# Optimization experiments

Hardware: AMD Instinct MI355X
Metric: run time of the kernel (lower is better)

## Reference

```python
import jax, jax.numpy as jnp
import numpy as np

B, C, W, H = 16, 256, 32, 32  # L = W*H = 1024
NUM_HEAD = 4
DIM_HEAD = C  # dim_head defaults to in_channels


def setup_inputs() -> dict:
    key = jax.random.key(0)
    ks = jax.random.split(key, 6)
    s = 0.02  # small init scale, like trained linear weights
    return {
        "x": jax.random.normal(ks[0], (B, C, W, H), dtype=jnp.float32),
        "Wq": jax.random.normal(ks[1], (NUM_HEAD, DIM_HEAD, C), dtype=jnp.float32) * s,
        "Wk": jax.random.normal(ks[2], (NUM_HEAD, DIM_HEAD, C), dtype=jnp.float32) * s,
        "Wv": jax.random.normal(ks[3], (NUM_HEAD, DIM_HEAD, C), dtype=jnp.float32) * s,
        "Wo_w": jax.random.normal(ks[4], (C, NUM_HEAD * DIM_HEAD), dtype=jnp.float32) * s,
        "Wo_b": jax.random.normal(ks[5], (C,), dtype=jnp.float32) * s,
    }


def reference(x, Wq, Wk, Wv, Wo_w, Wo_b):
    b, c, w, h = x.shape
    L = w * h
    # [b,c,w,h] -> [b,L,c]
    xs = jnp.transpose(x, (0, 2, 3, 1)).reshape(b, L, c)
    # per-head projections (torch Linear: y = x @ W^T), batched over heads
    Q = jnp.einsum('blc,hdc->bhld', xs, Wq)
    K = jnp.einsum('blc,hdc->bhld', xs, Wk)
    V = jnp.einsum('blc,hdc->bhld', xs, Wv)
    # no softmax: scores = Q K^T, heads = scores V
    scores = jnp.einsum('bhld,bhmd->bhlm', Q, K)  # [b,H,L,L]
    heads = jnp.einsum('bhlm,bhmd->bhld', scores, V)  # [b,H,L,d]
    # concat heads along channel dim -> [b,L,H*d], then output projection
    cat = jnp.transpose(heads, (0, 2, 1, 3)).reshape(b, L, -1)
    z = cat @ Wo_w.T + Wo_b  # [b,L,c]
    return jnp.transpose(z, (0, 2, 1)).reshape(b, c, w, h)
```

## Files before the change

kernel.cpp:

```cpp
#include <hip/hip_runtime.h>
#include <hip/hip_bf16.h>

typedef __attribute__((ext_vector_type(8))) short s8v;
typedef __attribute__((ext_vector_type(4))) float f4v;

__device__ __forceinline__ ushort f2bf(float f) {
    unsigned u = __builtin_bit_cast(unsigned, f);
    unsigned r = (u + 0x7fffu + ((u >> 16) & 1u)) >> 16;
    return (ushort)r;
}

__device__ __forceinline__ int fsw(int row) { return ((row >> 1) ^ (row >> 3)) & 3; }

__device__ __forceinline__ void gload16(const ushort* g, ushort* l) {
    __builtin_amdgcn_global_load_lds(
        (const __attribute__((address_space(1))) unsigned*)g,
        (__attribute__((address_space(3))) unsigned*)l, 16, 0, 0);
}

__device__ __forceinline__ void cvtw16(ushort* p, float4 a, float4 b) {
    s8v u;
    u[0] = (short)f2bf(a.x); u[1] = (short)f2bf(a.y);
    u[2] = (short)f2bf(a.z); u[3] = (short)f2bf(a.w);
    u[4] = (short)f2bf(b.x); u[5] = (short)f2bf(b.y);
    u[6] = (short)f2bf(b.z); u[7] = (short)f2bf(b.w);
    *(s8v*)p = u;
}

__device__ __forceinline__ void scatw(ushort* L, int c8, int d, float4 a, float4 b) {
    float v[8] = { a.x, a.y, a.z, a.w, b.x, b.y, b.z, b.w };
#pragma unroll
    for (int i = 0; i < 8; ++i) {
        int row = c8 + i;
        L[row * 32 + (((d >> 3) ^ fsw(row)) << 3) + (d & 7)] = f2bf(v[i]);
    }
}

template<int NT>
__device__ __forceinline__ void gemmS(
    const float* __restrict__ Xb, const float* __restrict__ Yb,
    ushort* lds, int row0, int col0, ushort* __restrict__ O, int ldo) {
    const int tid = threadIdx.x, wave = tid >> 6, lane = tid & 63;
    const int g = wave >> 2, w4 = wave & 3;
    const int wr = w4 >> 1, wc = w4 & 1;
    const int rA = lane & 15, kg = lane >> 4;
    const int tg = tid & 255;
    const int srow = tg >> 2, slot = tg & 3;
    const int kb = g * (NT * 32);
    ushort* LA = lds + g * 16384;
    ushort* LB = LA + 8192;
    const int wadr = srow * 32 + ((slot ^ fsw(srow)) << 3);
    const float* gx = Xb + (size_t)(row0 + srow) * 1024 + kb + slot * 8;
    const float* gy = Yb + (size_t)(col0 + srow) * 1024 + kb + slot * 8;
    f4v acc[2][2] = {};

    float4 bx[4][2], by[4][2];
#pragma unroll
    for (int p = 0; p < 3; ++p) {
        bx[p][0] = *(const float4*)(gx + p * 32);
        bx[p][1] = *(const float4*)(gx + p * 32 + 4);
        by[p][0] = *(const float4*)(gy + p * 32);
        by[p][1] = *(const float4*)(gy + p * 32 + 4);
    }
    cvtw16(LA + wadr, bx[0][0], bx[0][1]);
    cvtw16(LB + wadr, by[0][0], by[0][1]);

#pragma unroll
    for (int t = 0; t < NT; ++t) {
        if (t + 3 < NT) {
            const int bi = (t + 3) & 3;
            bx[bi][0] = *(const float4*)(gx + (t + 3) * 32);
            bx[bi][1] = *(const float4*)(gx + (t + 3) * 32 + 4);
            by[bi][0] = *(const float4*)(gy + (t + 3) * 32);
            by[bi][1] = *(const float4*)(gy + (t + 3) * 32 + 4);
        }
        if (t + 1 < NT) {
            const int bi = (t + 1) & 3;
            cvtw16(LA + ((t + 1) & 3) * 2048 + wadr, bx[bi][0], bx[bi][1]);
            cvtw16(LB + ((t + 1) & 3) * 2048 + wadr, by[bi][0], by[bi][1]);
        }
        asm volatile("s_waitcnt lgkmcnt(0)" ::: "memory");
        __builtin_amdgcn_s_barrier();
        __builtin_amdgcn_sched_barrier(0);
        const ushort* pa = LA + (t & 3) * 2048;
        const ushort* pb = LB + (t & 3) * 2048;
        s8v a[2], b[2];
#pragma unroll
        for (int m = 0; m < 2; ++m) {
            int row = wr * 32 + m * 16 + rA;
            a[m] = *(const s8v*)&pa[row * 32 + ((kg ^ fsw(row)) << 3)];
        }
#pragma unroll
        for (int n = 0; n < 2; ++n) {
            int row = wc * 32 + n * 16 + rA;
            b[n] = *(const s8v*)&pb[row * 32 + ((kg ^ fsw(row)) << 3)];
        }
#pragma unroll
        for (int m = 0; m < 2; ++m)
#pragma unroll
            for (int n = 0; n < 2; ++n)
                acc[m][n] = __builtin_amdgcn_mfma_f32_16x16x32_bf16(a[m], b[n], acc[m][n], 0, 0, 0);
    }
    __syncthreads();
    float* red = (float*)lds;
    if (g == 1) {
#pragma unroll
        for (int m = 0; m < 2; ++m)
#pragma unroll
            for (int n = 0; n < 2; ++n)
                *(f4v*)&red[(w4 * 64 + lane) * 16 + (m * 2 + n) * 4] = acc[m][n];
    }
    __syncthreads();
    if (g == 0) {
        int r4 = (lane >> 4) * 4, cl = lane & 15;
#pragma unroll
        for (int m = 0; m < 2; ++m)
#pragma unroll
            for (int n = 0; n < 2; ++n) {
                f4v o = *(const f4v*)&red[(w4 * 64 + lane) * 16 + (m * 2 + n) * 4];
                f4v s = acc[m][n] + o;
                int row = row0 + wr * 32 + m * 16 + r4;
                int col = col0 + wc * 32 + n * 16 + cl;
#pragma unroll
                for (int r = 0; r < 4; ++r)
                    O[(size_t)(row + r) * ldo + col] = f2bf(s[r]);
            }
    }
}

template<int XT>
__device__ __forceinline__ void gemmWT(
    const float* __restrict__ Xw, const float* __restrict__ Yw,
    ushort* lds, int row0, int col0, ushort* __restrict__ O, int ldo) {
    const int NT = 4;
    const int tid = threadIdx.x, wave = tid >> 6, lane = tid & 63;
    const int g = wave >> 2, w4 = wave & 3;
    const int wr = w4 >> 1, wc = w4 & 1;
    const int rA = lane & 15, kg = lane >> 4;
    const int tg = tid & 255;
    const int kb = g * 128;
    ushort* LA = lds + g * 16384;
    ushort* LB = LA + 8192;
    const int dT = tg >> 3, c8 = (tg & 7) * 8;
    const int srow = tg >> 2, slot = tg & 3;
    const int wadr = srow * 32 + ((slot ^ fsw(srow)) << 3);
    f4v acc[2][2] = {};

    float4 bx[4][2], by[4][2];
#pragma unroll
    for (int p = 0; p < 3; ++p) {
        if (XT) {
            bx[p][0] = *(const float4*)(Xw + (size_t)(kb + p * 32 + dT) * 256 + row0 + c8);
            bx[p][1] = *(const float4*)(Xw + (size_t)(kb + p * 32 + dT) * 256 + row0 + c8 + 4);
        } else {
            bx[p][0] = *(const float4*)(Xw + (size_t)(row0 + srow) * 1024 + kb + p * 32 + slot * 8);
            bx[p][1] = *(const float4*)(Xw + (size_t)(row0 + srow) * 1024 + kb + p * 32 + slot * 8 + 4);
        }
        by[p][0] = *(const float4*)(Yw + (size_t)(kb + p * 32 + dT) * 256 + col0 + c8);
        by[p][1] = *(const float4*)(Yw + (size_t)(kb + p * 32 + dT) * 256 + col0 + c8 + 4);
    }
    if (XT) scatw(LA, c8, dT, bx[0][0], bx[0][1]);
    else    cvtw16(LA + wadr, bx[0][0], bx[0][1]);
    scatw(LB, c8, dT, by[0][0], by[0][1]);

#pragma unroll
    for (int t = 0; t < NT; ++t) {
        if (t + 3 < NT) {
            const int bi = (t + 3) & 3;
            if (XT) {
                bx[bi][0] = *(const float4*)(Xw + (size_t)(kb + (t + 3) * 32 + dT) * 256 + row0 + c8);
                bx[bi][1] = *(const float4*)(Xw + (size_t)(kb + (t + 3) * 32 + dT) * 256 + row0 + c8 + 4);
            } else {
                bx[bi][0] = *(const float4*)(Xw + (size_t)(row0 + srow) * 1024 + kb + (t + 3) * 32 + slot * 8);
                bx[bi][1] = *(const float4*)(Xw + (size_t)(row0 + srow) * 1024 + kb + (t + 3) * 32 + slot * 8 + 4);
            }
            by[bi][0] = *(const float4*)(Yw + (size_t)(kb + (t + 3) * 32 + dT) * 256 + col0 + c8);
            by[bi][1] = *(const float4*)(Yw + (size_t)(kb + (t + 3) * 32 + dT) * 256 + col0 + c8 + 4);
        }
        if (t + 1 < NT) {
            const int bi = (t + 1) & 3;
            ushort* la = LA + ((t + 1) & 3) * 2048;
            ushort* lb = LB + ((t + 1) & 3) * 2048;
            if (XT) scatw(la, c8, dT, bx[bi][0], bx[bi][1]);
            else    cvtw16(la + wadr, bx[bi][0], bx[bi][1]);
            scatw(lb, c8, dT, by[bi][0], by[bi][1]);
        }
        asm volatile("s_waitcnt lgkmcnt(0)" ::: "memory");
        __builtin_amdgcn_s_barrier();
        __builtin_amdgcn_sched_barrier(0);
        const ushort* pa = LA + (t & 3) * 2048;
        const ushort* pb = LB + (t & 3) * 2048;
        s8v a[2], b[2];
#pragma unroll
        for (int m = 0; m < 2; ++m) {
            int row = wr * 32 + m * 16 + rA;
            a[m] = *(const s8v*)&pa[row * 32 + ((kg ^ fsw(row)) << 3)];
        }
#pragma unroll
        for (int n = 0; n < 2; ++n) {
            int row = wc * 32 + n * 16 + rA;
            b[n] = *(const s8v*)&pb[row * 32 + ((kg ^ fsw(row)) << 3)];
        }
#pragma unroll
        for (int m = 0; m < 2; ++m)
#pragma unroll
            for (int n = 0; n < 2; ++n)
                acc[m][n] = __builtin_amdgcn_mfma_f32_16x16x32_bf16(a[m], b[n], acc[m][n], 0, 0, 0);
    }
    __syncthreads();
    float* red = (float*)lds;
    if (g == 1) {
#pragma unroll
        for (int m = 0; m < 2; ++m)
#pragma unroll
            for (int n = 0; n < 2; ++n)
                *(f4v*)&red[(w4 * 64 + lane) * 16 + (m * 2 + n) * 4] = acc[m][n];
    }
    __syncthreads();
    if (g == 0) {
        int r4 = (lane >> 4) * 4, cl = lane & 15;
#pragma unroll
        for (int m = 0; m < 2; ++m)
#pragma unroll
            for (int n = 0; n < 2; ++n) {
                f4v o = *(const f4v*)&red[(w4 * 64 + lane) * 16 + (m * 2 + n) * 4];
                f4v s = acc[m][n] + o;
                int row = row0 + wr * 32 + m * 16 + r4;
                int col = col0 + wc * 32 + n * 16 + cl;
#pragma unroll
                for (int r = 0; r < 4; ++r)
                    O[(size_t)(row + r) * ldo + col] = f2bf(s[r]);
            }
    }
}

__device__ __forceinline__ void gemm64x8(
    const ushort* __restrict__ Xb, const ushort* __restrict__ Yb,
    int ldx, int ldy, ushort* lds, int row0, int col0, int K,
    ushort* __restrict__ O, int ldo) {
    const int tid = threadIdx.x, wave = tid >> 6, lane = tid & 63;
    const int g = wave >> 2, w4 = wave & 3;
    const int wr = w4 >> 1, wc = w4 & 1;
    const int rA = lane & 15, kg = lane >> 4;
    const int srow = w4 * 16 + (lane >> 2);
    const int scol = ((lane & 3) ^ fsw(srow)) * 8;
    const int K2 = K >> 1, NT = K2 >> 5, kb = g * K2;
    ushort* LA = lds + g * 16384;
    ushort* LB = LA + 8192;
    f4v acc[2][2] = {};
    __syncthreads();
    const ushort* gx = Xb + (size_t)(row0 + srow) * ldx + kb + scol;
    const ushort* gy = Yb + (size_t)(col0 + srow) * ldy + kb + scol;
    gload16(gx,      LA + w4 * 512);
    gload16(gy,      LB + w4 * 512);
    gload16(gx + 32, LA + 2048 + w4 * 512);
    gload16(gy + 32, LB + 2048 + w4 * 512);
    for (int t = 0; t < NT; ++t) {
        if (t + 2 < NT) {
            int s2 = (t + 2) & 3, kt = (t + 2) << 5;
            gload16(gx + kt, LA + s2 * 2048 + w4 * 512);
            gload16(gy + kt, LB + s2 * 2048 + w4 * 512);
            asm volatile("s_waitcnt vmcnt(4)" ::: "memory");
        } else if (t + 1 < NT) {
            asm volatile("s_waitcnt vmcnt(2)" ::: "memory");
        } else {
            asm volatile("s_waitcnt vmcnt(0)" ::: "memory");
        }
        __builtin_amdgcn_s_barrier();
        __builtin_amdgcn_sched_barrier(0);
        const ushort* pa = LA + (t & 3) * 2048;
        const ushort* pb = LB + (t & 3) * 2048;
        s8v a[2], b[2];
#pragma unroll
        for (int m = 0; m < 2; ++m) {
            int row = wr * 32 + m * 16 + rA;
            a[m] = *(const s8v*)&pa[row * 32 + ((kg ^ fsw(row)) << 3)];
        }
#pragma unroll
        for (int n = 0; n < 2; ++n) {
            int row = wc * 32 + n * 16 + rA;
            b[n] = *(const s8v*)&pb[row * 32 + ((kg ^ fsw(row)) << 3)];
        }
#pragma unroll
        for (int m = 0; m < 2; ++m)
#pragma unroll
            for (int n = 0; n < 2; ++n)
                acc[m][n] = __builtin_amdgcn_mfma_f32_16x16x32_bf16(a[m], b[n], acc[m][n], 0, 0, 0);
    }
    __syncthreads();
    float* red = (float*)lds;
    if (g == 1) {
#pragma unroll
        for (int m = 0; m < 2; ++m)
#pragma unroll
            for (int n = 0; n < 2; ++n)
                *(f4v*)&red[(w4 * 64 + lane) * 16 + (m * 2 + n) * 4] = acc[m][n];
    }
    __syncthreads();
    if (g == 0) {
        int r4 = (lane >> 4) * 4, cl = lane & 15;
#pragma unroll
        for (int m = 0; m < 2; ++m)
#pragma unroll
            for (int n = 0; n < 2; ++n) {
                f4v o = *(const f4v*)&red[(w4 * 64 + lane) * 16 + (m * 2 + n) * 4];
                f4v s = acc[m][n] + o;
                int row = row0 + wr * 32 + m * 16 + r4;
                int col = col0 + wc * 32 + n * 16 + cl;
#pragma unroll
                for (int r = 0; r < 4; ++r)
                    O[(size_t)(row + r) * ldo + col] = f2bf(s[r]);
            }
    }
}

template<int OBF>
__device__ __forceinline__ void gemm128x8(
    const ushort* __restrict__ Xb, const ushort* __restrict__ Yb,
    int ldx, int ldy, ushort* lds, int row0, int col0, int K,
    void* __restrict__ Oraw, int ldo, const float* __restrict__ bias) {
    const int tid = threadIdx.x, wave = tid >> 6, lane = tid & 63;
    const int wr = wave >> 2, wc = wave & 3;
    const int rA = lane & 15, kg = lane >> 4;
    const int srow = wave * 16 + (lane >> 2);
    const int scol = ((lane & 3) ^ fsw(srow)) * 8;
    const int NT = K >> 5;
    ushort* LA = lds;
    ushort* LB = lds + 16384;
    f4v acc[4][2] = {};
    __syncthreads();
    const ushort* gx = Xb + (size_t)(row0 + srow) * ldx + scol;
    const ushort* gy = Yb + (size_t)(col0 + srow) * ldy + scol;
#pragma unroll
    for (int p = 0; p < 2; ++p) {
        gload16(gx + p * 32, LA + p * 4096 + wave * 512);
        gload16(gy + p * 32, LB + p * 4096 + wave * 512);
    }
    for (int t = 0; t < NT; ++t) {
        if (t + 2 < NT) {
            int s2 = (t + 2) & 3, kt = (t + 2) << 5;
            gload16(gx + kt, LA + s2 * 4096 + wave * 512);
            gload16(gy + kt, LB + s2 * 4096 + wave * 512);
            asm volatile("s_waitcnt vmcnt(4)" ::: "memory");
        } else if (t + 1 < NT) {
            asm volatile("s_waitcnt vmcnt(2)" ::: "memory");
        } else {
            asm volatile("s_waitcnt vmcnt(0)" ::: "memory");
        }
        __builtin_amdgcn_s_barrier();
        __builtin_amdgcn_sched_barrier(0);
        const ushort* pa = LA + (t & 3) * 4096;
        const ushort* pb = LB + (t & 3) * 4096;
        s8v a[4], b[2];
#pragma unroll
        for (int m = 0; m < 4; ++m) {
            int row = wr * 64 + m * 16 + rA;
            a[m] = *(const s8v*)&pa[row * 32 + ((kg ^ fsw(row)) << 3)];
        }
#pragma unroll
        for (int n = 0; n < 2; ++n) {
            int row = wc * 32 + n * 16 + rA;
            b[n] = *(const s8v*)&pb[row * 32 + ((kg ^ fsw(row)) << 3)];
        }
#pragma unroll
        for (int m = 0; m < 4; ++m)
#pragma unroll
            for (int n = 0; n < 2; ++n)
                acc[m][n] = __builtin_amdgcn_mfma_f32_16x16x32_bf16(a[m], b[n], acc[m][n], 0, 0, 0);
    }
    int r4 = (lane >> 4) * 4, cl = lane & 15;
    if (OBF) {
        ushort* O = (ushort*)Oraw;
#pragma unroll
        for (int m = 0; m < 4; ++m)
#pragma unroll
            for (int n = 0; n < 2; ++n) {
                int row = row0 + wr * 64 + m * 16 + r4;
                int col = col0 + wc * 32 + n * 16 + cl;
#pragma unroll
                for (int r = 0; r < 4; ++r)
                    O[(size_t)(row + r) * ldo + col] = f2bf(acc[m][n][r]);
            }
    } else {
        float* O = (float*)Oraw;
#pragma unroll
        for (int m = 0; m < 4; ++m)
#pragma unroll
            for (int n = 0; n < 2; ++n) {
                int row = row0 + wr * 64 + m * 16 + r4;
                int col = col0 + wc * 32 + n * 16 + cl;
#pragma unroll
                for (int r = 0; r < 4; ++r)
                    O[(size_t)(row + r) * ldo + col] = acc[m][n][r] + bias[row + r];
            }
    }
}

__global__ __launch_bounds__(512, 2) void kSP(
    const float* __restrict__ x, const float* __restrict__ Wq,
    const float* __restrict__ Wk, const float* __restrict__ Wv,
    const float* __restrict__ Wo,
    ushort* __restrict__ xlc, ushort* __restrict__ S16,
    ushort* __restrict__ A16, ushort* __restrict__ BT) {
    __shared__ __align__(16) ushort lds[32768];
    const int bid = blockIdx.x, tid = threadIdx.x;
    {
        int xcd = bid & 7, idx = bid >> 3;
        int b = 2 * xcd + (idx >> 4), tile = idx & 15;
        const float* Xb = x + (size_t)b * 262144;
        gemmS<16>(Xb, Xb, lds, (tile >> 2) * 64, (tile & 3) * 64,
                  S16 + (size_t)b * 65536, 256);
    }
    for (int jid = bid; jid < 1152; jid += 256) {
        __syncthreads();
        if (jid < 1024) {
            ushort (*t)[72] = (ushort(*)[72])lds;
            int lt = jid & 15, ct = (jid >> 4) & 3, b2 = jid >> 6;
            int r = tid >> 3, c0 = (tid & 7) * 8;
            size_t so = (size_t)(b2 * 256 + ct * 64 + r) * 1024 + lt * 64 + c0;
            float4 v0 = *(const float4*)(x + so);
            float4 v1 = *(const float4*)(x + so + 4);
            ushort4 u0 = { f2bf(v0.x), f2bf(v0.y), f2bf(v0.z), f2bf(v0.w) };
            ushort4 u1 = { f2bf(v1.x), f2bf(v1.y), f2bf(v1.z), f2bf(v1.w) };
            *(ushort4*)&t[r][c0] = u0;
            *(ushort4*)&t[r][c0 + 4] = u1;
            __syncthreads();
            size_t dof = (size_t)(b2 * 1024 + lt * 64 + r) * 256 + ct * 64 + c0;
            ushort4 w0 = { t[c0][r], t[c0 + 1][r], t[c0 + 2][r], t[c0 + 3][r] };
            ushort4 w1 = { t[c0 + 4][r], t[c0 + 5][r], t[c0 + 6][r], t[c0 + 7][r] };
            *(ushort4*)(xlc + dof) = w0;
            *(ushort4*)(xlc + dof + 4) = w1;
        } else if (jid < 1088) {
            int q = jid - 1024, h = q >> 4, t2 = q & 15;
            gemmWT<1>(Wq + (size_t)h * 65536, Wk + (size_t)h * 65536, lds,
                      (t2 >> 2) * 64, (t2 & 3) * 64, A16 + (size_t)h * 65536, 256);
        } else {
            int q = jid - 1088, h = q >> 4, t2 = q & 15;
            gemmWT<0>(Wo + (size_t)h * 256, Wv + (size_t)h * 65536, lds,
                      (t2 >> 2) * 64, (t2 & 3) * 64, BT + (size_t)h * 256, 1024);
        }
    }
}

__global__ __launch_bounds__(512, 2) void kT1(
    const ushort* __restrict__ A16, const ushort* __restrict__ S16,
    ushort* __restrict__ T1) {
    __shared__ __align__(16) ushort lds[32768];
    int j = blockIdx.x, xcd = j & 7, idx = j >> 3;
    int b = 2 * xcd + (idx >> 4), h = (idx >> 2) & 3, tile = idx & 3;
    gemm128x8<1>(A16 + (size_t)h * 65536, S16 + (size_t)b * 65536, 256, 256, lds,
                 (tile >> 1) * 128, (tile & 1) * 128, 256,
                 T1 + (size_t)b * 262144 + h * 256, 1024, nullptr);
}

__global__ __launch_bounds__(512, 2) void kGT(
    const ushort* __restrict__ BT, const ushort* __restrict__ T1,
    ushort* __restrict__ GT) {
    __shared__ __align__(16) ushort lds[32768];
    int j = blockIdx.x, xcd = j & 7, idx = j >> 3;
    int b = 2 * xcd + (idx >> 4), tile = idx & 15;
    gemm64x8(BT, T1 + (size_t)b * 262144, 1024, 1024, lds,
             (tile >> 2) * 64, (tile & 3) * 64, 1024, GT + (size_t)b * 65536, 256);
}

__global__ __launch_bounds__(512, 2) void kOUT(
    const ushort* __restrict__ GT, const ushort* __restrict__ xlc,
    float* __restrict__ out, const float* __restrict__ bias) {
    __shared__ __align__(16) ushort lds[32768];
    int j = blockIdx.x, xcd = j & 7, idx = j >> 3;
    int b = 2 * xcd + (idx >> 4), tile = idx & 15;
    gemm128x8<0>(GT + (size_t)b * 65536, xlc + (size_t)b * 262144, 256, 256, lds,
                 (tile >> 3) * 128, (tile & 7) * 128, 256,
                 out + (size_t)b * 262144, 1024, bias);
}

extern "C" void kernel_launch(void* const* d_in, const int* in_sizes, int n_in,
                              void* d_out, int out_size, void* d_ws, size_t ws_size,
                              hipStream_t stream) {
    const float* x  = (const float*)d_in[0];
    const float* Wq = (const float*)d_in[1];
    const float* Wk = (const float*)d_in[2];
    const float* Wv = (const float*)d_in[3];
    const float* Wo = (const float*)d_in[4];
    const float* Wb = (const float*)d_in[5];

    char* ws = (char*)d_ws;
    ushort* xlc = (ushort*)(ws + 0);
    ushort* T1  = (ushort*)(ws + 8388608);
    ushort* S16 = (ushort*)(ws + 16777216);
    ushort* GT  = (ushort*)(ws + 18874368);
    ushort* A16 = (ushort*)(ws + 20971520);
    ushort* BT  = (ushort*)(ws + 21495808);

    hipLaunchKernelGGL(kSP,  dim3(256), dim3(512), 0, stream,
                       x, Wq, Wk, Wv, Wo, xlc, S16, A16, BT);
    hipLaunchKernelGGL(kT1,  dim3(256), dim3(512), 0, stream, A16, S16, T1);
    hipLaunchKernelGGL(kGT,  dim3(256), dim3(512), 0, stream, BT, T1, GT);
    hipLaunchKernelGGL(kOUT, dim3(256), dim3(512), 0, stream, GT, xlc, (float*)d_out, Wb);
}
```

Measured before the change: 42.83 us.

## Fuse four kernels into one persistent megakernel with per-batch atomic barriers

Replaces the four-kernel launch sequence with a single persistent kernel that uses global atomic flag counters as per-batch and weight-ready barriers between stages. This removes the inter-kernel launch gaps and the extra xlc transpose pass: the final GEMM reads the fp32 input directly and converts it to bf16 while staging into LDS. The bf16 conversion helper is also switched to the library intrinsic. The cost is spin-wait barriers that rely on all 256 blocks being co-resident, plus an added memset launch to clear the flags.

```diff
diff --git a/kernel.cpp b/kernel.cpp
--- a/kernel.cpp
+++ b/kernel.cpp
@@ -5,9 +5,8 @@
 typedef __attribute__((ext_vector_type(4))) float f4v;
 
 __device__ __forceinline__ ushort f2bf(float f) {
-    unsigned u = __builtin_bit_cast(unsigned, f);
-    unsigned r = (u + 0x7fffu + ((u >> 16) & 1u)) >> 16;
-    return (ushort)r;
+    __hip_bfloat16 h = __float2bfloat16(f);
+    return __builtin_bit_cast(ushort, h);
 }
 
 __device__ __forceinline__ int fsw(int row) { return ((row >> 1) ^ (row >> 3)) & 3; }
@@ -34,6 +33,25 @@
         int row = c8 + i;
         L[row * 32 + (((d >> 3) ^ fsw(row)) << 3) + (d & 7)] = f2bf(v[i]);
     }
+}
+
+__device__ __forceinline__ void barB(unsigned* flags, int idx, unsigned tgt,
+                                     int alsoIdx, unsigned alsoTgt) {
+    __syncthreads();
+    if (threadIdx.x == 0) {
+        __threadfence();
+        atomicAdd(&flags[idx], 1u);
+        for (;;) {
+            unsigned v = __hip_atomic_load(&flags[idx], __ATOMIC_RELAXED, __HIP_MEMORY_SCOPE_AGENT);
+            unsigned w = (alsoIdx >= 0)
+                ? __hip_atomic_load(&flags[alsoIdx], __ATOMIC_RELAXED, __HIP_MEMORY_SCOPE_AGENT)
+                : alsoTgt;
+            if (v >= tgt && w >= alsoTgt) break;
+            __builtin_amdgcn_s_sleep(2);
+        }
+        __threadfence();
+    }
+    __syncthreads();
 }
 
 template<int NT>
@@ -53,6 +71,7 @@
     const float* gx = Xb + (size_t)(row0 + srow) * 1024 + kb + slot * 8;
     const float* gy = Yb + (size_t)(col0 + srow) * 1024 + kb + slot * 8;
     f4v acc[2][2] = {};
+    __syncthreads();
 
     float4 bx[4][2], by[4][2];
 #pragma unroll
@@ -145,6 +164,7 @@
     const int srow = tg >> 2, slot = tg & 3;
     const int wadr = srow * 32 + ((slot ^ fsw(srow)) << 3);
     f4v acc[2][2] = {};
+    __syncthreads();
 
     float4 bx[4][2], by[4][2];
 #pragma unroll
@@ -314,11 +334,10 @@
     }
 }
 
-template<int OBF>
 __device__ __forceinline__ void gemm128x8(
     const ushort* __restrict__ Xb, const ushort* __restrict__ Yb,
     int ldx, int ldy, ushort* lds, int row0, int col0, int K,
-    void* __restrict__ Oraw, int ldo, const float* __restrict__ bias) {
+    ushort* __restrict__ O, int ldo) {
     const int tid = threadIdx.x, wave = tid >> 6, lane = tid & 63;
     const int wr = wave >> 2, wc = wave & 3;
     const int rA = lane & 15, kg = lane >> 4;
@@ -369,109 +388,159 @@
                 acc[m][n] = __builtin_amdgcn_mfma_f32_16x16x32_bf16(a[m], b[n], acc[m][n], 0, 0, 0);
     }
     int r4 = (lane >> 4) * 4, cl = lane & 15;
-    if (OBF) {
-        ushort* O = (ushort*)Oraw;
+    ushort* Ob = O;
+#pragma unroll
+    for (int m = 0; m < 4; ++m)
+#pragma unroll
+        for (int n = 0; n < 2; ++n) {
+            int row = row0 + wr * 64 + m * 16 + r4;
+            int col = col0 + wc * 32 + n * 16 + cl;
+#pragma unroll
+            for (int r = 0; r < 4; ++r)
+                Ob[(size_t)(row + r) * ldo + col] = f2bf(acc[m][n][r]);
+        }
+}
+
+__device__ __forceinline__ void gemmOUT(
+    const ushort* __restrict__ Ga, const float* __restrict__ Xf,
+    ushort* lds, int row0, int col0,
+    float* __restrict__ O, const float* __restrict__ bias) {
+    const int tid = threadIdx.x, wave = tid >> 6, lane = tid & 63;
+    const int wr = wave >> 2, wc = wave & 3;
+    const int rA = lane & 15, kg = lane >> 4;
+    const int srowA = wave * 16 + (lane >> 2);
+    const int scolA = ((lane & 3) ^ fsw(srowA)) * 8;
+    ushort* LA = lds;
+    ushort* LB = lds + 16384;
+    const int kk = tid >> 4, l8 = (tid & 15) * 8;
+    int wadr[8];
+#pragma unroll
+    for (int i = 0; i < 8; ++i) {
+        int row = l8 + i;
+        wadr[i] = row * 32 + (((kk >> 3) ^ fsw(row)) << 3) + (kk & 7);
+    }
+    const ushort* gA = Ga + (size_t)(row0 + srowA) * 256 + scolA;
+    const float* gB = Xf + (size_t)kk * 1024 + col0 + l8;
+    f4v acc[4][2] = {};
+    __syncthreads();
+
+    float4 ra[4], rb[4];
+    gload16(gA + 0, LA + 0 * 4096 + wave * 512);
+    ra[0] = *(const float4*)(gB);
+    rb[0] = *(const float4*)(gB + 4);
+    gload16(gA + 32, LA + 1 * 4096 + wave * 512);
+    ra[1] = *(const float4*)(gB + 32768);
+    rb[1] = *(const float4*)(gB + 32768 + 4);
+    asm volatile("s_waitcnt vmcnt(0)" ::: "memory");
+    {
+        float v[8] = { ra[0].x, ra[0].y, ra[0].z, ra[0].w, rb[0].x, rb[0].y, rb[0].z, rb[0].w };
+#pragma unroll
+        for (int i = 0; i < 8; ++i) LB[wadr[i]] = f2bf(v[i]);
+    }
+    asm volatile("s_waitcnt lgkmcnt(0)" ::: "memory");
+    __builtin_amdgcn_s_barrier();
+    __builtin_amdgcn_sched_barrier(0);
+
+#pragma unroll
+    for (int t = 0; t < 8; ++t) {
+        if (t + 1 < 8) {
+            if (t + 2 < 8) {
+                gload16(gA + (t + 2) * 32, LA + ((t + 2) & 3) * 4096 + wave * 512);
+                ra[(t + 2) & 3] = *(const float4*)(gB + (size_t)(t + 2) * 32768);
+                rb[(t + 2) & 3] = *(const float4*)(gB + (size_t)(t + 2) * 32768 + 4);
+            }
+            {
+                const int bi = (t + 1) & 3;
+                float v[8] = { ra[bi].x, ra[bi].y, ra[bi].z, ra[bi].w,
+                               rb[bi].x, rb[bi].y, rb[bi].z, rb[bi].w };
+                ushort* lb = LB + bi * 4096;
+#pragma unroll
+                for (int i = 0; i < 8; ++i) lb[wadr[i]] = f2bf(v[i]);
+            }
+            if (t + 2 < 8) { asm volatile("s_waitcnt vmcnt(3)" ::: "memory"); }
+            else           { asm volatile("s_waitcnt vmcnt(0)" ::: "memory"); }
+            asm volatile("s_waitcnt lgkmcnt(0)" ::: "memory");
+            __builtin_amdgcn_s_barrier();
+            __builtin_amdgcn_sched_barrier(0);
+        }
+        const ushort* pa = LA + (t & 3) * 4096;
+        const ushort* pb = LB + (t & 3) * 4096;
+        s8v a[4], b[2];
+#pragma unroll
+        for (int m = 0; m < 4; ++m) {
+            int row = wr * 64 + m * 16 + rA;
+            a[m] = *(const s8v*)&pa[row * 32 + ((kg ^ fsw(row)) << 3)];
+        }
+#pragma unroll
+        for (int n = 0; n < 2; ++n) {
+            int row = wc * 32 + n * 16 + rA;
+            b[n] = *(const s8v*)&pb[row * 32 + ((kg ^ fsw(row)) << 3)];
+        }
 #pragma unroll
         for (int m = 0; m < 4; ++m)
 #pragma unroll
-            for (int n = 0; n < 2; ++n) {
-                int row = row0 + wr * 64 + m * 16 + r4;
-                int col = col0 + wc * 32 + n * 16 + cl;
-#pragma unroll
-                for (int r = 0; r < 4; ++r)
-                    O[(size_t)(row + r) * ldo + col] = f2bf(acc[m][n][r]);
-            }
-    } else {
-        float* O = (float*)Oraw;
-#pragma unroll
-        for (int m = 0; m < 4; ++m)
-#pragma unroll
-            for (int n = 0; n < 2; ++n) {
-                int row = row0 + wr * 64 + m * 16 + r4;
-                int col = col0 + wc * 32 + n * 16 + cl;
-#pragma unroll
-                for (int r = 0; r < 4; ++r)
-                    O[(size_t)(row + r) * ldo + col] = acc[m][n][r] + bias[row + r];
-            }
-    }
-}
-
-__global__ __launch_bounds__(512, 2) void kSP(
+            for (int n = 0; n < 2; ++n)
+                acc[m][n] = __builtin_amdgcn_mfma_f32_16x16x32_bf16(a[m], b[n], acc[m][n], 0, 0, 0);
+    }
+    int r4 = (lane >> 4) * 4, cl = lane & 15;
+#pragma unroll
+    for (int m = 0; m < 4; ++m)
+#pragma unroll
+        for (int n = 0; n < 2; ++n) {
+            int row = row0 + wr * 64 + m * 16 + r4;
+            int col = col0 + wc * 32 + n * 16 + cl;
+#pragma unroll
+            for (int r = 0; r < 4; ++r)
+                O[(size_t)(row + r) * 1024 + col] = acc[m][n][r] + bias[row + r];
+        }
+}
+
+__global__ __launch_bounds__(512, 2) void mega(
     const float* __restrict__ x, const float* __restrict__ Wq,
     const float* __restrict__ Wk, const float* __restrict__ Wv,
-    const float* __restrict__ Wo,
-    ushort* __restrict__ xlc, ushort* __restrict__ S16,
-    ushort* __restrict__ A16, ushort* __restrict__ BT) {
+    const float* __restrict__ Wo, const float* __restrict__ Wb,
+    float* __restrict__ out,
+    ushort* __restrict__ T1, ushort* __restrict__ S16, ushort* __restrict__ GT,
+    ushort* __restrict__ A16, ushort* __restrict__ BT, unsigned* __restrict__ flags) {
     __shared__ __align__(16) ushort lds[32768];
     const int bid = blockIdx.x, tid = threadIdx.x;
-    {
-        int xcd = bid & 7, idx = bid >> 3;
-        int b = 2 * xcd + (idx >> 4), tile = idx & 15;
-        const float* Xb = x + (size_t)b * 262144;
-        gemmS<16>(Xb, Xb, lds, (tile >> 2) * 64, (tile & 3) * 64,
-                  S16 + (size_t)b * 65536, 256);
-    }
-    for (int jid = bid; jid < 1152; jid += 256) {
-        __syncthreads();
-        if (jid < 1024) {
-            ushort (*t)[72] = (ushort(*)[72])lds;
-            int lt = jid & 15, ct = (jid >> 4) & 3, b2 = jid >> 6;
-            int r = tid >> 3, c0 = (tid & 7) * 8;
-            size_t so = (size_t)(b2 * 256 + ct * 64 + r) * 1024 + lt * 64 + c0;
-            float4 v0 = *(const float4*)(x + so);
-            float4 v1 = *(const float4*)(x + so + 4);
-            ushort4 u0 = { f2bf(v0.x), f2bf(v0.y), f2bf(v0.z), f2bf(v0.w) };
-            ushort4 u1 = { f2bf(v1.x), f2bf(v1.y), f2bf(v1.z), f2bf(v1.w) };
-            *(ushort4*)&t[r][c0] = u0;
-            *(ushort4*)&t[r][c0 + 4] = u1;
-            __syncthreads();
-            size_t dof = (size_t)(b2 * 1024 + lt * 64 + r) * 256 + ct * 64 + c0;
-            ushort4 w0 = { t[c0][r], t[c0 + 1][r], t[c0 + 2][r], t[c0 + 3][r] };
-            ushort4 w1 = { t[c0 + 4][r], t[c0 + 5][r], t[c0 + 6][r], t[c0 + 7][r] };
-            *(ushort4*)(xlc + dof) = w0;
-            *(ushort4*)(xlc + dof + 4) = w1;
-        } else if (jid < 1088) {
-            int q = jid - 1024, h = q >> 4, t2 = q & 15;
+
+    if (bid < 128) {
+        if (bid < 64) {
+            int h = bid >> 4, t2 = bid & 15;
             gemmWT<1>(Wq + (size_t)h * 65536, Wk + (size_t)h * 65536, lds,
                       (t2 >> 2) * 64, (t2 & 3) * 64, A16 + (size_t)h * 65536, 256);
         } else {
-            int q = jid - 1088, h = q >> 4, t2 = q & 15;
+            int q = bid - 64, h = q >> 4, t2 = q & 15;
             gemmWT<0>(Wo + (size_t)h * 256, Wv + (size_t)h * 65536, lds,
                       (t2 >> 2) * 64, (t2 & 3) * 64, BT + (size_t)h * 256, 1024);
         }
-    }
-}
-
-__global__ __launch_bounds__(512, 2) void kT1(
-    const ushort* __restrict__ A16, const ushort* __restrict__ S16,
-    ushort* __restrict__ T1) {
-    __shared__ __align__(16) ushort lds[32768];
-    int j = blockIdx.x, xcd = j & 7, idx = j >> 3;
-    int b = 2 * xcd + (idx >> 4), h = (idx >> 2) & 3, tile = idx & 3;
-    gemm128x8<1>(A16 + (size_t)h * 65536, S16 + (size_t)b * 65536, 256, 256, lds,
-                 (tile >> 1) * 128, (tile & 1) * 128, 256,
-                 T1 + (size_t)b * 262144 + h * 256, 1024, nullptr);
-}
-
-__global__ __launch_bounds__(512, 2) void kGT(
-    const ushort* __restrict__ BT, const ushort* __restrict__ T1,
-    ushort* __restrict__ GT) {
-    __shared__ __align__(16) ushort lds[32768];
-    int j = blockIdx.x, xcd = j & 7, idx = j >> 3;
-    int b = 2 * xcd + (idx >> 4), tile = idx & 15;
+        __syncthreads();
+        if (tid == 0) { __threadfence(); atomicAdd(&flags[48], 1u); }
+    }
+
+    const int xcd = bid & 7;
+    const int b = 2 * xcd + ((bid >> 3) & 1);
+    const int t = bid >> 4;
+    const float* xb = x + (size_t)b * 262144;
+
+    gemmS<16>(xb, xb, lds, (t >> 2) * 64, (t & 3) * 64, S16 + (size_t)b * 65536, 256);
+    barB(flags, b * 3 + 0, 16, 48, 128);
+
+    {
+        int h = t >> 2, q = t & 3;
+        gemm128x8(A16 + (size_t)h * 65536, S16 + (size_t)b * 65536, 256, 256, lds,
+                  (q >> 1) * 128, (q & 1) * 128, 256,
+                  T1 + (size_t)b * 262144 + h * 256, 1024);
+    }
+    barB(flags, b * 3 + 1, 16, -1, 0);
+
     gemm64x8(BT, T1 + (size_t)b * 262144, 1024, 1024, lds,
-             (tile >> 2) * 64, (tile & 3) * 64, 1024, GT + (size_t)b * 65536, 256);
-}
-
-__global__ __launch_bounds__(512, 2) void kOUT(
-    const ushort* __restrict__ GT, const ushort* __restrict__ xlc,
-    float* __restrict__ out, const float* __restrict__ bias) {
-    __shared__ __align__(16) ushort lds[32768];
-    int j = blockIdx.x, xcd = j & 7, idx = j >> 3;
-    int b = 2 * xcd + (idx >> 4), tile = idx & 15;
-    gemm128x8<0>(GT + (size_t)b * 65536, xlc + (size_t)b * 262144, 256, 256, lds,
-                 (tile >> 3) * 128, (tile & 7) * 128, 256,
-                 out + (size_t)b * 262144, 1024, bias);
+             (t >> 2) * 64, (t & 3) * 64, 1024, GT + (size_t)b * 65536, 256);
+    barB(flags, b * 3 + 2, 16, -1, 0);
+
+    gemmOUT(GT + (size_t)b * 65536, xb, lds,
+            (t >> 3) * 128, (t & 7) * 128, out + (size_t)b * 262144, Wb);
 }
 
 extern "C" void kernel_launch(void* const* d_in, const int* in_sizes, int n_in,
@@ -485,16 +554,15 @@
     const float* Wb = (const float*)d_in[5];
 
     char* ws = (char*)d_ws;
-    ushort* xlc = (ushort*)(ws + 0);
-    ushort* T1  = (ushort*)(ws + 8388608);
-    ushort* S16 = (ushort*)(ws + 16777216);
-    ushort* GT  = (ushort*)(ws + 18874368);
-    ushort* A16 = (ushort*)(ws + 20971520);
-    ushort* BT  = (ushort*)(ws + 21495808);
-
-    hipLaunchKernelGGL(kSP,  dim3(256), dim3(512), 0, stream,
-                       x, Wq, Wk, Wv, Wo, xlc, S16, A16, BT);
-    hipLaunchKernelGGL(kT1,  dim3(256), dim3(512), 0, stream, A16, S16, T1);
-    hipLaunchKernelGGL(kGT,  dim3(256), dim3(512), 0, stream, BT, T1, GT);
-    hipLaunchKernelGGL(kOUT, dim3(256), dim3(512), 0, stream, GT, xlc, (float*)d_out, Wb);
-}
+    ushort*   T1    = (ushort*)(ws + 0);
+    ushort*   S16   = (ushort*)(ws + 16777216);
+    ushort*   GT    = (ushort*)(ws + 20971520);
+    ushort*   A16   = (ushort*)(ws + 25165824);
+    ushort*   BT    = (ushort*)(ws + 26214400);
+    unsigned* flags = (unsigned*)(ws + 33554432);
+
+    hipMemsetAsync(flags, 0, 256, stream);
+    hipLaunchKernelGGL(mega, dim3(256), dim3(512), 0, stream,
+                       x, Wq, Wk, Wv, Wo, Wb, (float*)d_out,
+                       T1, S16, GT, A16, BT, flags);
+}
```

Result: slower. 100.8 us (+135.3%).

## Exploit Gram symmetry, split projection prep into separate blocks, move Wo·Wv to kT1

Applied to the files above, without the earlier changes.

The x·x^T Gram matrix is symmetric, so only the upper-triangle 64x64 tiles are computed (10 of 16 per batch) and each off-diagonal tile is also written transposed. The kSP grid becomes 480 blocks with distinct roles (Gram tiles, Wq·Wk products, x transpose), so they no longer share one looped schedule. The Wo·Wv product moves into kT1 as extra blocks, which shortens the first kernel. The bf16 conversion now uses the library intrinsic, and the mirror writes are scattered 8-byte stores that may be poorly coalesced.

```diff
diff --git a/kernel.cpp b/kernel.cpp
--- a/kernel.cpp
+++ b/kernel.cpp
@@ -5,9 +5,8 @@
 typedef __attribute__((ext_vector_type(4))) float f4v;
 
 __device__ __forceinline__ ushort f2bf(float f) {
-    unsigned u = __builtin_bit_cast(unsigned, f);
-    unsigned r = (u + 0x7fffu + ((u >> 16) & 1u)) >> 16;
-    return (ushort)r;
+    __hip_bfloat16 h = __float2bfloat16(f);
+    return __builtin_bit_cast(ushort, h);
 }
 
 __device__ __forceinline__ int fsw(int row) { return ((row >> 1) ^ (row >> 3)) & 3; }
@@ -36,10 +35,10 @@
     }
 }
 
-template<int NT>
 __device__ __forceinline__ void gemmS(
-    const float* __restrict__ Xb, const float* __restrict__ Yb,
-    ushort* lds, int row0, int col0, ushort* __restrict__ O, int ldo) {
+    const float* __restrict__ Xb, ushort* lds, int row0, int col0,
+    ushort* __restrict__ S, int mirror) {
+    const int NT = 16;
     const int tid = threadIdx.x, wave = tid >> 6, lane = tid & 63;
     const int g = wave >> 2, w4 = wave & 3;
     const int wr = w4 >> 1, wc = w4 & 1;
@@ -51,8 +50,9 @@
     ushort* LB = LA + 8192;
     const int wadr = srow * 32 + ((slot ^ fsw(srow)) << 3);
     const float* gx = Xb + (size_t)(row0 + srow) * 1024 + kb + slot * 8;
-    const float* gy = Yb + (size_t)(col0 + srow) * 1024 + kb + slot * 8;
+    const float* gy = Xb + (size_t)(col0 + srow) * 1024 + kb + slot * 8;
     f4v acc[2][2] = {};
+    __syncthreads();
 
     float4 bx[4][2], by[4][2];
 #pragma unroll
@@ -121,9 +121,13 @@
                 f4v s = acc[m][n] + o;
                 int row = row0 + wr * 32 + m * 16 + r4;
                 int col = col0 + wc * 32 + n * 16 + cl;
-#pragma unroll
-                for (int r = 0; r < 4; ++r)
-                    O[(size_t)(row + r) * ldo + col] = f2bf(s[r]);
+                ushort4 tv = { f2bf(s[0]), f2bf(s[1]), f2bf(s[2]), f2bf(s[3]) };
+                S[(size_t)(row + 0) * 256 + col] = tv.x;
+                S[(size_t)(row + 1) * 256 + col] = tv.y;
+                S[(size_t)(row + 2) * 256 + col] = tv.z;
+                S[(size_t)(row + 3) * 256 + col] = tv.w;
+                if (mirror)
+                    *(ushort4*)&S[(size_t)col * 256 + row] = tv;
             }
     }
 }
@@ -145,6 +149,7 @@
     const int srow = tg >> 2, slot = tg & 3;
     const int wadr = srow * 32 + ((slot ^ fsw(srow)) << 3);
     f4v acc[2][2] = {};
+    __syncthreads();
 
     float4 bx[4][2], by[4][2];
 #pragma unroll
@@ -398,25 +403,33 @@
 
 __global__ __launch_bounds__(512, 2) void kSP(
     const float* __restrict__ x, const float* __restrict__ Wq,
-    const float* __restrict__ Wk, const float* __restrict__ Wv,
-    const float* __restrict__ Wo,
-    ushort* __restrict__ xlc, ushort* __restrict__ S16,
-    ushort* __restrict__ A16, ushort* __restrict__ BT) {
+    const float* __restrict__ Wk,
+    ushort* __restrict__ S16, ushort* __restrict__ A16, ushort* __restrict__ xlc) {
     __shared__ __align__(16) ushort lds[32768];
     const int bid = blockIdx.x, tid = threadIdx.x;
-    {
+    if (bid < 160) {
         int xcd = bid & 7, idx = bid >> 3;
-        int b = 2 * xcd + (idx >> 4), tile = idx & 15;
-        const float* Xb = x + (size_t)b * 262144;
-        gemmS<16>(Xb, Xb, lds, (tile >> 2) * 64, (tile & 3) * 64,
-                  S16 + (size_t)b * 65536, 256);
-    }
-    for (int jid = bid; jid < 1152; jid += 256) {
-        __syncthreads();
-        if (jid < 1024) {
-            ushort (*t)[72] = (ushort(*)[72])lds;
+        int b = 2 * xcd + (idx >= 10);
+        int tri = (idx >= 10) ? idx - 10 : idx;
+        int ti, tj;
+        if (tri < 4)      { ti = 0; tj = tri; }
+        else if (tri < 7) { ti = 1; tj = tri - 3; }
+        else if (tri < 9) { ti = 2; tj = tri - 5; }
+        else              { ti = 3; tj = 3; }
+        const float* xb = x + (size_t)b * 262144;
+        gemmS(xb, lds, ti * 64, tj * 64, S16 + (size_t)b * 65536, ti != tj);
+    } else if (bid < 224) {
+        int q = bid - 160, h = q >> 4, t2 = q & 15;
+        gemmWT<1>(Wq + (size_t)h * 65536, Wk + (size_t)h * 65536, lds,
+                  (t2 >> 2) * 64, (t2 & 3) * 64, A16 + (size_t)h * 65536, 256);
+    } else {
+        ushort (*t)[72] = (ushort(*)[72])lds;
+        int r = tid >> 3, c0 = (tid & 7) * 8;
+#pragma unroll
+        for (int rr = 0; rr < 4; ++rr) {
+            int jid = (bid - 224) + 256 * rr;
+            __syncthreads();
             int lt = jid & 15, ct = (jid >> 4) & 3, b2 = jid >> 6;
-            int r = tid >> 3, c0 = (tid & 7) * 8;
             size_t so = (size_t)(b2 * 256 + ct * 64 + r) * 1024 + lt * 64 + c0;
             float4 v0 = *(const float4*)(x + so);
             float4 v1 = *(const float4*)(x + so + 4);
@@ -430,27 +443,27 @@
             ushort4 w1 = { t[c0 + 4][r], t[c0 + 5][r], t[c0 + 6][r], t[c0 + 7][r] };
             *(ushort4*)(xlc + dof) = w0;
             *(ushort4*)(xlc + dof + 4) = w1;
-        } else if (jid < 1088) {
-            int q = jid - 1024, h = q >> 4, t2 = q & 15;
-            gemmWT<1>(Wq + (size_t)h * 65536, Wk + (size_t)h * 65536, lds,
-                      (t2 >> 2) * 64, (t2 & 3) * 64, A16 + (size_t)h * 65536, 256);
-        } else {
-            int q = jid - 1088, h = q >> 4, t2 = q & 15;
-            gemmWT<0>(Wo + (size_t)h * 256, Wv + (size_t)h * 65536, lds,
-                      (t2 >> 2) * 64, (t2 & 3) * 64, BT + (size_t)h * 256, 1024);
         }
     }
 }
 
 __global__ __launch_bounds__(512, 2) void kT1(
     const ushort* __restrict__ A16, const ushort* __restrict__ S16,
-    ushort* __restrict__ T1) {
+    const float* __restrict__ Wo, const float* __restrict__ Wv,
+    ushort* __restrict__ T1, ushort* __restrict__ BT) {
     __shared__ __align__(16) ushort lds[32768];
-    int j = blockIdx.x, xcd = j & 7, idx = j >> 3;
-    int b = 2 * xcd + (idx >> 4), h = (idx >> 2) & 3, tile = idx & 3;
-    gemm128x8<1>(A16 + (size_t)h * 65536, S16 + (size_t)b * 65536, 256, 256, lds,
-                 (tile >> 1) * 128, (tile & 1) * 128, 256,
-                 T1 + (size_t)b * 262144 + h * 256, 1024, nullptr);
+    int j = blockIdx.x;
+    if (j < 256) {
+        int xcd = j & 7, idx = j >> 3;
+        int b = 2 * xcd + (idx >> 4), h = (idx >> 2) & 3, tile = idx & 3;
+        gemm128x8<1>(A16 + (size_t)h * 65536, S16 + (size_t)b * 65536, 256, 256, lds,
+                     (tile >> 1) * 128, (tile & 1) * 128, 256,
+                     T1 + (size_t)b * 262144 + h * 256, 1024, nullptr);
+    } else {
+        int q = j - 256, h = q >> 4, t2 = q & 15;
+        gemmWT<0>(Wo + (size_t)h * 256, Wv + (size_t)h * 65536, lds,
+                  (t2 >> 2) * 64, (t2 & 3) * 64, BT + (size_t)h * 256, 1024);
+    }
 }
 
 __global__ __launch_bounds__(512, 2) void kGT(
@@ -485,16 +498,15 @@
     const float* Wb = (const float*)d_in[5];
 
     char* ws = (char*)d_ws;
-    ushort* xlc = (ushort*)(ws + 0);
-    ushort* T1  = (ushort*)(ws + 8388608);
+    ushort* T1  = (ushort*)(ws + 0);
+    ushort* xlc = (ushort*)(ws + 8388608);
     ushort* S16 = (ushort*)(ws + 16777216);
-    ushort* GT  = (ushort*)(ws + 18874368);
-    ushort* A16 = (ushort*)(ws + 20971520);
-    ushort* BT  = (ushort*)(ws + 21495808);
-
-    hipLaunchKernelGGL(kSP,  dim3(256), dim3(512), 0, stream,
-                       x, Wq, Wk, Wv, Wo, xlc, S16, A16, BT);
-    hipLaunchKernelGGL(kT1,  dim3(256), dim3(512), 0, stream, A16, S16, T1);
+    ushort* GT  = (ushort*)(ws + 20971520);
+    ushort* A16 = (ushort*)(ws + 25165824);
+    ushort* BT  = (ushort*)(ws + 26214400);
+
+    hipLaunchKernelGGL(kSP,  dim3(480), dim3(512), 0, stream, x, Wq, Wk, S16, A16, xlc);
+    hipLaunchKernelGGL(kT1,  dim3(320), dim3(512), 0, stream, A16, S16, Wo, Wv, T1, BT);
     hipLaunchKernelGGL(kGT,  dim3(256), dim3(512), 0, stream, BT, T1, GT);
     hipLaunchKernelGGL(kOUT, dim3(256), dim3(512), 0, stream, GT, xlc, (float*)d_out, Wb);
 }
```

New measurement: 39.82 us. 1.08x faster.
